# Performance work log

Hardware: AMD Instinct MI355X
Metric: run time of the kernel (lower is better)

The kernel has to match this reference:

```python
import jax, jax.numpy as jnp
import numpy as np

IN_CH = 12      # InChannels global in original code
GROWTH = 12     # growth global == growthRate
H = 34          # peptide/pseudo-sequence length (long==34 branch)
BN_EPS = 1e-5


def setup_inputs() -> dict:
    key = jax.random.key(0)
    k = jax.random.split(key, 5)
    B, C = 16384, 72  # C = IN_CH + 5*GROWTH
    x = jax.random.normal(k[0], (B, C, H, 1), dtype=jnp.float32)
    gamma = jnp.ones((C,), dtype=jnp.float32)
    beta = jnp.zeros((C,), dtype=jnp.float32)
    conv_w = jax.random.normal(k[1], (GROWTH, C, 3, 1), dtype=jnp.float32) * 0.05
    fc_w = jax.random.normal(k[2], (1, H), dtype=jnp.float32)
    fc_bias = jax.random.normal(k[3], (1,), dtype=jnp.float32)
    return {"x": x, "gamma": gamma, "beta": beta, "conv_w": conv_w,
            "fc_w": fc_w, "fc_bias": fc_bias}


def reference(x, gamma, beta, conv_w, fc_w, fc_bias):
    B, C, Hh, Ww = x.shape
    n = (C - IN_CH) // GROWTH  # number of growth groups
    sg = jax.lax.stop_gradient

    x1 = x[:, :IN_CH]                                 # [B,12,H,1]
    x2g = x[:, IN_CH:].reshape(B, n, GROWTH, Hh, 1)    # [B,n,g,H,1]

    # per-group channel means, squeezed over the width-1 axis -> [B,n,H]
    m = x2g.mean(axis=2)[..., 0]
    x11 = x1.mean(axis=1)[..., 0]                      # [B,H]

    w = fc_w[0]                                        # [H]
    lin_m = m @ w + fc_bias[0]                         # [B,n]  (bias included per F.linear call)
    lin_out = lin_m[:, -1]                             # lin(x_outt), [B]
    lin_x11 = x11 @ w + fc_bias[0]                     # [B]

    # gate for x1: sigmoid(lin(x_outt) + lin(x11)); note bias appears twice, as in torch
    g1 = jax.nn.sigmoid(lin_out + lin_x11)             # [B]
    # gates for groups 0..n-2: sigmoid(lin(group_i) + lin(x_outt))
    gates = jax.nn.sigmoid(lin_m[:, :-1] + lin_out[:, None])  # [B,n-1]

    # the expand/repeat/view dance collapses to a per-sample scalar gate broadcast
    x1g = g1[:, None, None, None] * sg(x1)             # x1 is detached in original
    # groups are appended in reversed order (i = n-2 .. 0)
    gg = gates[:, ::-1][:, :, None, None, None] * sg(x2g[:, :-1][:, ::-1])
    gg_flat = gg.reshape(B, (n - 1) * GROWTH, Hh, 1)
    x_out = x2g[:, -1]                                 # last group, appended ungated

    xxx = jnp.concatenate([x1g, gg_flat, x_out], axis=1)  # [B,C,H,1]

    # BatchNorm2d in training mode (batch statistics, biased variance)
    mu = xxx.mean(axis=(0, 2, 3), keepdims=True)
    var = xxx.var(axis=(0, 2, 3), keepdims=True)
    xn = (xxx - mu) * jax.lax.rsqrt(var + BN_EPS)
    h = jax.nn.relu(gamma[None, :, None, None] * xn + beta[None, :, None, None])

    # Conv2d(C -> GROWTH, kernel (3,1), padding (1,0), no bias)
    out = jax.lax.conv_general_dilated(
        h, conv_w, window_strides=(1, 1), padding=((1, 1), (0, 0)),
        dimension_numbers=("NCHW", "OIHW", "NCHW"))

    return jnp.concatenate([x, out], axis=1)           # [B, C+GROWTH, H, 1]
```

## Files before the change

### kernel.cpp

```cpp
#include <hip/hip_runtime.h>
#include <hip/hip_fp16.h>
#include <math.h>


#define BN_EPS 1e-5f

#define WS_S    0
#define WS_SS   72
#define WS_A    144
#define WS_B    216
#define WS_WT   288
#define WS_GATE 3744
#define K1_BLOCKS 512

typedef _Float16 f16x8 __attribute__((ext_vector_type(8)));
typedef float f32x4 __attribute__((ext_vector_type(4)));

__device__ __forceinline__ float sigmoidf_(float z) { return 1.f / (1.f + expf(-z)); }

__global__ __launch_bounds__(256) void k1_stats(const float* __restrict__ x,
                                                const float* __restrict__ fw,
                                                const float* __restrict__ fb,
                                                float* __restrict__ ws,
                                                float* __restrict__ part,
                                                int B, int nTrip)
{
    __shared__ float rs_s[3][72], rss_s[3][72], wsum_s[3][72];
    __shared__ float lm_s[3][6];
    __shared__ float sc_s[3][8];
    __shared__ float Sacc[144];

    const int tid = threadIdx.x;
    const int g = tid / 72;
    const int c = tid - g * 72;
    if (tid < 144) Sacc[tid] = 0.f;

    for (int t = blockIdx.x; t < nTrip; t += K1_BLOCKS) {
        const int b0 = t * 3;

        if (tid < 216 && b0 + g < B) {
            const float2* p = (const float2*)(x + (size_t)(b0 + g) * 2448 + c * 34);
            float rs = 0.f, rss = 0.f, wsm = 0.f;
#pragma unroll
            for (int i = 0; i < 17; ++i) {
                float2 v = p[i];
                rs += v.x + v.y;
                rss = fmaf(v.x, v.x, fmaf(v.y, v.y, rss));
                wsm = fmaf(v.x, fw[2 * i], fmaf(v.y, fw[2 * i + 1], wsm));
            }
            rs_s[g][c] = rs; rss_s[g][c] = rss; wsum_s[g][c] = wsm;
        }
        __syncthreads();

        if (tid < 18) {
            int gg = tid / 6, r = tid - gg * 6;
            float s = 0.f;
#pragma unroll
            for (int k = 0; k < 12; ++k) s += wsum_s[gg][r * 12 + k];
            lm_s[gg][r] = s * (1.f / 12.f) + fb[0];
        }
        __syncthreads();

        if (tid < 3 && b0 + tid < B) {
            float lin_out = lm_s[tid][5];
            float sc[6];
            sc[0] = sigmoidf_(lin_out + lm_s[tid][0]);
            sc[1] = sigmoidf_(lm_s[tid][4] + lin_out);
            sc[2] = sigmoidf_(lm_s[tid][3] + lin_out);
            sc[3] = sigmoidf_(lm_s[tid][2] + lin_out);
            sc[4] = sigmoidf_(lm_s[tid][1] + lin_out);
            sc[5] = 1.f;
            float* gb = ws + WS_GATE + (size_t)(b0 + tid) * 6;
#pragma unroll
            for (int r = 0; r < 6; ++r) { sc_s[tid][r] = sc[r]; gb[r] = sc[r]; }
        }
        __syncthreads();

        if (tid < 72) {
            const int r = tid / 12;
            const int dd[6] = {0, 36, 12, -12, -36, 0};
            const int src = tid + dd[r];
            float a = 0.f, q = 0.f;
#pragma unroll
            for (int gg = 0; gg < 3; ++gg) {
                if (b0 + gg < B) {
                    float s = sc_s[gg][r];
                    a = fmaf(s, rs_s[gg][src], a);
                    q = fmaf(s * s, rss_s[gg][src], q);
                }
            }
            Sacc[tid] += a; Sacc[72 + tid] += q;
        }
        __syncthreads();
    }

    if (tid < 144) part[(size_t)tid * K1_BLOCKS + blockIdx.x] = Sacc[tid];
}

__global__ __launch_bounds__(256) void k2a_reduce(float* __restrict__ ws,
                                                  const float* __restrict__ part)
{
    const int ch = blockIdx.x;
    const float* p = part + (size_t)ch * K1_BLOCKS;
    float s = 0.f;
    for (int i = threadIdx.x; i < K1_BLOCKS; i += 256) s += p[i];
#pragma unroll
    for (int off = 32; off; off >>= 1) s += __shfl_down(s, off, 64);
    __shared__ float wsum[4];
    if ((threadIdx.x & 63) == 0) wsum[threadIdx.x >> 6] = s;
    __syncthreads();
    if (threadIdx.x == 0) ws[WS_S + ch] = wsum[0] + wsum[1] + wsum[2] + wsum[3];
}

__global__ void k2b_finalize(const float* __restrict__ gamma,
                             const float* __restrict__ beta,
                             const float* __restrict__ cw,
                             float* __restrict__ ws, float invN)
{
    const int tid = threadIdx.x;
    if (tid < 72) {
        float S = ws[WS_S + tid], SS = ws[WS_SS + tid];
        float mu = S * invN;
        float var = SS * invN - mu * mu;
        float inv = rsqrtf(var + BN_EPS);
        float A = gamma[tid] * inv;
        ws[WS_A + tid] = A;
        ws[WS_B + tid] = beta[tid] - mu * A;
    }
    __half* wa = (__half*)(ws + WS_WT);
    for (int i = tid; i < 9 * 64 * 8; i += 256) {
        int j = i & 7;
        int lane = (i >> 3) & 63;
        int frag = i >> 9;
        int shift = frag / 3, ks = frag - shift * 3;
        int o = lane & 15, grp = lane >> 4;
        int ct = ks * 32 + grp * 8 + j;
        float v = (o < 12 && ct < 72) ? cw[o * 216 + ct * 3 + shift] : 0.f;
        wa[i] = __float2half(v);
    }
}

__global__ __launch_bounds__(256) void k3_out(const float* __restrict__ x,
                                              const float* __restrict__ ws,
                                              float* __restrict__ out, int B)
{
    __shared__ __align__(16) __half hs[6 * 2456];
    __shared__ float2 AB[73];
    __shared__ float gl[6][8];

    const int tid = threadIdx.x;
    const int lane = tid & 63;
    const int wid = tid >> 6;
    const int b0 = blockIdx.x * 6;
    int nb = B - b0; if (nb > 6) nb = 6;

    const __half* wa = (const __half*)(ws + WS_WT);
    f16x8 wA[9];
#pragma unroll
    for (int f = 0; f < 9; ++f)
        wA[f] = *(const f16x8*)(wa + (f * 64 + lane) * 8);

    if (tid < 73)
        AB[tid] = (tid < 72) ? make_float2(ws[WS_A + tid], ws[WS_B + tid])
                             : make_float2(0.f, 0.f);
    for (int t2 = tid; t2 < nb * 6; t2 += 256) {
        int g = t2 / 6, j = t2 - g * 6;
        gl[g][j] = ws[WS_GATE + (size_t)(b0 + g) * 6 + j];
    }
    if (tid < 24) {
        int g = tid >> 2, k = tid & 3;
        ((unsigned int*)hs)[g * 1228 + ((k < 2) ? k : (1224 + k))] = 0u;
    }
    if (nb < 6) {
        for (int i = tid; i < (6 - nb) * 1228; i += 256)
            ((unsigned int*)hs)[nb * 1228 + i] = 0u;
    }
    __syncthreads();

    for (int idx = tid; idx < nb * 612; idx += 256) {
        int g = idx / 612, v4 = idx - g * 612;
        size_t b = (size_t)(b0 + g);
        float4 q = ((const float4*)(x + b * 2448))[v4];
        ((float4*)(out + b * 2856))[v4] = q;

        const int ddc[6]  = {0, 36, 12, -12, -36, 0};
        const int sidx[6] = {0, 4, 3, 2, 1, 5};
        int rx = v4 / 102;
        int e  = v4 * 4;
        int cx0 = e / 34;
        int h0i = e - cx0 * 34;
        int dd  = ddc[rx];
        int cd0 = cx0 + dd;
        float2 ab0 = AB[cd0];
        float2 ab1 = AB[cd0 + 1];
        float s = gl[g][sidx[rx]];
        float vv[4] = {q.x, q.y, q.z, q.w};
        __half hv[4];
#pragma unroll
        for (int j = 0; j < 4; ++j) {
            float2 ab = (h0i + j >= 34) ? ab1 : ab0;
            hv[j] = __float2half(fmaxf(fmaf(ab.x * s, vv[j], ab.y), 0.f));
        }
        union { __half2 h2; unsigned int u; } pa, pb;
        pa.h2 = __halves2half2(hv[0], hv[1]);
        pb.h2 = __halves2half2(hv[2], hv[3]);
        int dst = g * 2456 + 4 + e + dd * 34;
        *reinterpret_cast<uint2*>(&hs[dst]) = make_uint2(pa.u, pb.u);
    }
    __syncthreads();

    const int sub = lane & 15, grp = lane >> 4;
    for (int t = wid; t < 13; t += 4) {
        const bool tail = (t == 12);
        int g, col;
        if (!tail) { g = t >> 1; col = (t & 1) * 16 + sub; }
        else       { g = (sub < 12) ? (sub >> 1) : 0; col = 32 + (sub & 1); }
        if (!tail && g >= nb) continue;

        const __half* hb = &hs[g * 2456 + 4];
        f32x4 acc = {0.f, 0.f, 0.f, 0.f};
        f16x8 save0, save1, save2;
        const bool needc = tail || ((t & 1) == 0);
        const int  csh   = tail ? 2 : 0;

#pragma unroll
        for (int ks = 0; ks < 3; ++ks) {
            const int cb = (ks < 2) ? (ks * 32 + grp * 8) : 64;
            const __half* hc = hb + cb * 34 + col;
#pragma unroll
            for (int sh = 0; sh < 3; ++sh) {
                f16x8 bf;
#pragma unroll
                for (int j = 0; j < 8; ++j)
                    ((unsigned short*)&bf)[j] =
                        *(const unsigned short*)(hc + j * 34 + (sh - 1));
                if (needc && sh == csh) {
                    if (ks == 0) save0 = bf;
                    else if (ks == 1) save1 = bf;
                    else save2 = bf;
                }
                acc = __builtin_amdgcn_mfma_f32_16x16x32_f16(
                          wA[sh * 3 + ks], bf, acc, 0, 0, 0);
            }
        }

        if (needc) {
            const bool m = tail ? (((sub & 1) == 1) && sub < 12) : (sub == 0);
#pragma unroll
            for (int ks = 0; ks < 3; ++ks) {
                const f16x8& sv = (ks == 0) ? save0 : (ks == 1) ? save1 : save2;
                f16x8 bt;
#pragma unroll
                for (int w = 0; w < 4; ++w)
                    ((unsigned int*)&bt)[w] =
                        m ? (((const unsigned int*)&sv)[w] ^ 0x80008000u) : 0u;
                acc = __builtin_amdgcn_mfma_f32_16x16x32_f16(
                          wA[csh * 3 + ks], bt, acc, 0, 0, 0);
            }
        }

        const bool gok = tail ? (sub < 12 && g < nb) : true;
        if (gok) {
            float* op = out + (size_t)(b0 + g) * 2856 + 2448 + col;
#pragma unroll
            for (int j = 0; j < 4; ++j) {
                int o = grp * 4 + j;
                if (o < 12) op[o * 34] = acc[j];
            }
        }
    }
}

extern "C" void kernel_launch(void* const* d_in, const int* in_sizes, int n_in,
                              void* d_out, int out_size, void* d_ws, size_t ws_size,
                              hipStream_t stream)
{
    const float* x     = (const float*)d_in[0];
    const float* gamma = (const float*)d_in[1];
    const float* beta  = (const float*)d_in[2];
    const float* cw    = (const float*)d_in[3];
    const float* fw    = (const float*)d_in[4];
    const float* fb    = (const float*)d_in[5];
    float* out = (float*)d_out;
    float* ws  = (float*)d_ws;

    const int B = in_sizes[0] / (72 * 34);
    const int nTrip = (B + 2) / 3;
    float* part = ws + WS_GATE + (size_t)B * 6;

    k1_stats<<<K1_BLOCKS, 256, 0, stream>>>(x, fw, fb, ws, part, B, nTrip);
    k2a_reduce<<<144, 256, 0, stream>>>(ws, part);
    k2b_finalize<<<1, 256, 0, stream>>>(gamma, beta, cw, ws, 1.f / ((float)B * 34.f));
    k3_out<<<(B + 5) / 6, 256, 0, stream>>>(x, ws, out, B);
}
```

Baseline: 387.3 us.

## Stage stats input via coalesced LDS loads, merge finalize kernel, enlarge grid

The stats kernel now copies each triplet of samples into shared memory with coalesced float4 loads before the per-channel reductions, replacing strided float2 global reads. The grid grows from 512 to up to 1024 blocks, capped by workspace size. The single-block finalize kernel is removed: the weight repacking moves into extra blocks of the reduce kernel, and the BN scale and shift are computed per block in the output kernel. This drops one launch and serial tail, at the cost of extra shared memory in the stats kernel and redundant per-block BN math.

```diff
diff --git a/kernel.cpp b/kernel.cpp
--- a/kernel.cpp
+++ b/kernel.cpp
@@ -7,11 +7,8 @@
 
 #define WS_S    0
 #define WS_SS   72
-#define WS_A    144
-#define WS_B    216
 #define WS_WT   288
 #define WS_GATE 3744
-#define K1_BLOCKS 512
 
 typedef _Float16 f16x8 __attribute__((ext_vector_type(8)));
 typedef float f32x4 __attribute__((ext_vector_type(4)));
@@ -25,6 +22,7 @@
                                                 float* __restrict__ part,
                                                 int B, int nTrip)
 {
+    __shared__ float xs[3 * 2448];
     __shared__ float rs_s[3][72], rss_s[3][72], wsum_s[3][72];
     __shared__ float lm_s[3][6];
     __shared__ float sc_s[3][8];
@@ -35,11 +33,20 @@
     const int c = tid - g * 72;
     if (tid < 144) Sacc[tid] = 0.f;
 
-    for (int t = blockIdx.x; t < nTrip; t += K1_BLOCKS) {
+    for (int t = blockIdx.x; t < nTrip; t += gridDim.x) {
         const int b0 = t * 3;
-
-        if (tid < 216 && b0 + g < B) {
-            const float2* p = (const float2*)(x + (size_t)(b0 + g) * 2448 + c * 34);
+        int nbt = B - b0; if (nbt > 3) nbt = 3;
+
+        {
+            const float4* xp = (const float4*)(x + (size_t)b0 * 2448);
+            const int nf4 = nbt * 612;
+            for (int i = tid; i < nf4; i += 256)
+                ((float4*)xs)[i] = xp[i];
+        }
+        __syncthreads();
+
+        if (tid < 216 && g < nbt) {
+            const float2* p = (const float2*)(xs + (g * 72 + c) * 34);
             float rs = 0.f, rss = 0.f, wsm = 0.f;
 #pragma unroll
             for (int i = 0; i < 17; ++i) {
@@ -83,7 +90,7 @@
             float a = 0.f, q = 0.f;
 #pragma unroll
             for (int gg = 0; gg < 3; ++gg) {
-                if (b0 + gg < B) {
+                if (gg < nbt) {
                     float s = sc_s[gg][r];
                     a = fmaf(s, rs_s[gg][src], a);
                     q = fmaf(s * s, rss_s[gg][src], q);
@@ -94,55 +101,77 @@
         __syncthreads();
     }
 
-    if (tid < 144) part[(size_t)tid * K1_BLOCKS + blockIdx.x] = Sacc[tid];
+    if (tid < 144) part[(size_t)tid * gridDim.x + blockIdx.x] = Sacc[tid];
 }
 
 __global__ __launch_bounds__(256) void k2a_reduce(float* __restrict__ ws,
-                                                  const float* __restrict__ part)
-{
-    const int ch = blockIdx.x;
-    const float* p = part + (size_t)ch * K1_BLOCKS;
-    float s = 0.f;
-    for (int i = threadIdx.x; i < K1_BLOCKS; i += 256) s += p[i];
-#pragma unroll
-    for (int off = 32; off; off >>= 1) s += __shfl_down(s, off, 64);
-    __shared__ float wsum[4];
-    if ((threadIdx.x & 63) == 0) wsum[threadIdx.x >> 6] = s;
-    __syncthreads();
-    if (threadIdx.x == 0) ws[WS_S + ch] = wsum[0] + wsum[1] + wsum[2] + wsum[3];
-}
-
-__global__ void k2b_finalize(const float* __restrict__ gamma,
-                             const float* __restrict__ beta,
-                             const float* __restrict__ cw,
-                             float* __restrict__ ws, float invN)
-{
-    const int tid = threadIdx.x;
-    if (tid < 72) {
-        float S = ws[WS_S + tid], SS = ws[WS_SS + tid];
-        float mu = S * invN;
-        float var = SS * invN - mu * mu;
-        float inv = rsqrtf(var + BN_EPS);
-        float A = gamma[tid] * inv;
-        ws[WS_A + tid] = A;
-        ws[WS_B + tid] = beta[tid] - mu * A;
-    }
-    __half* wa = (__half*)(ws + WS_WT);
-    for (int i = tid; i < 9 * 64 * 8; i += 256) {
-        int j = i & 7;
-        int lane = (i >> 3) & 63;
-        int frag = i >> 9;
-        int shift = frag / 3, ks = frag - shift * 3;
-        int o = lane & 15, grp = lane >> 4;
-        int ct = ks * 32 + grp * 8 + j;
-        float v = (o < 12 && ct < 72) ? cw[o * 216 + ct * 3 + shift] : 0.f;
-        wa[i] = __float2half(v);
-    }
+                                                  const float* __restrict__ part,
+                                                  const float* __restrict__ cw,
+                                                  int nblk)
+{
+    const int bid = blockIdx.x;
+    if (bid < 144) {
+        const float* p = part + (size_t)bid * nblk;
+        float s = 0.f;
+        for (int i = threadIdx.x; i < nblk; i += 256) s += p[i];
+#pragma unroll
+        for (int off = 32; off; off >>= 1) s += __shfl_down(s, off, 64);
+        __shared__ float wsum[4];
+        if ((threadIdx.x & 63) == 0) wsum[threadIdx.x >> 6] = s;
+        __syncthreads();
+        if (threadIdx.x == 0) ws[WS_S + bid] = wsum[0] + wsum[1] + wsum[2] + wsum[3];
+    } else {
+        __half* wa = (__half*)(ws + WS_WT);
+        const int base = (bid - 144) * 512;
+        for (int i = base + threadIdx.x; i < base + 512; i += 256) {
+            int j = i & 7;
+            int lane = (i >> 3) & 63;
+            int frag = i >> 9;
+            int shift = frag / 3, ks = frag - shift * 3;
+            int o = lane & 15, grp = lane >> 4;
+            int ct = ks * 32 + grp * 8 + j;
+            float v = (o < 12 && ct < 72) ? cw[o * 216 + ct * 3 + shift] : 0.f;
+            wa[i] = __float2half(v);
+        }
+    }
+}
+
+__device__ __forceinline__ void pack_h(int g, int v4, float4 q,
+                                       const float2* __restrict__ ABs,
+                                       const float* __restrict__ glf,
+                                       __half* __restrict__ hs)
+{
+    const int ddc[6]  = {0, 36, 12, -12, -36, 0};
+    const int sidx[6] = {0, 4, 3, 2, 1, 5};
+    int rx = v4 / 102;
+    int e  = v4 * 4;
+    int cx0 = e / 34;
+    int h0i = e - cx0 * 34;
+    int dd  = ddc[rx];
+    int cd0 = cx0 + dd;
+    float2 ab0 = ABs[cd0];
+    float2 ab1 = ABs[cd0 + 1];
+    float s = glf[g * 8 + sidx[rx]];
+    float vv[4] = {q.x, q.y, q.z, q.w};
+    __half hv[4];
+#pragma unroll
+    for (int j = 0; j < 4; ++j) {
+        float2 ab = (h0i + j >= 34) ? ab1 : ab0;
+        hv[j] = __float2half(fmaxf(fmaf(ab.x * s, vv[j], ab.y), 0.f));
+    }
+    union { __half2 h2; unsigned int u; } pa, pb;
+    pa.h2 = __halves2half2(hv[0], hv[1]);
+    pb.h2 = __halves2half2(hv[2], hv[3]);
+    int dst = g * 2456 + 4 + e + dd * 34;
+    *reinterpret_cast<uint2*>(&hs[dst]) = make_uint2(pa.u, pb.u);
 }
 
 __global__ __launch_bounds__(256) void k3_out(const float* __restrict__ x,
                                               const float* __restrict__ ws,
-                                              float* __restrict__ out, int B)
+                                              const float* __restrict__ gamma,
+                                              const float* __restrict__ beta,
+                                              float* __restrict__ out, int B,
+                                              float invN)
 {
     __shared__ __align__(16) __half hs[6 * 2456];
     __shared__ float2 AB[73];
@@ -160,9 +189,18 @@
     for (int f = 0; f < 9; ++f)
         wA[f] = *(const f16x8*)(wa + (f * 64 + lane) * 8);
 
-    if (tid < 73)
-        AB[tid] = (tid < 72) ? make_float2(ws[WS_A + tid], ws[WS_B + tid])
-                             : make_float2(0.f, 0.f);
+    if (tid < 73) {
+        if (tid < 72) {
+            float S = ws[WS_S + tid], SS = ws[WS_SS + tid];
+            float mu = S * invN;
+            float var = SS * invN - mu * mu;
+            float inv = rsqrtf(var + BN_EPS);
+            float A = gamma[tid] * inv;
+            AB[tid] = make_float2(A, beta[tid] - mu * A);
+        } else {
+            AB[72] = make_float2(0.f, 0.f);
+        }
+    }
     for (int t2 = tid; t2 < nb * 6; t2 += 256) {
         int g = t2 / 6, j = t2 - g * 6;
         gl[g][j] = ws[WS_GATE + (size_t)(b0 + g) * 6 + j];
@@ -177,35 +215,15 @@
     }
     __syncthreads();
 
-    for (int idx = tid; idx < nb * 612; idx += 256) {
-        int g = idx / 612, v4 = idx - g * 612;
-        size_t b = (size_t)(b0 + g);
-        float4 q = ((const float4*)(x + b * 2448))[v4];
-        ((float4*)(out + b * 2856))[v4] = q;
-
-        const int ddc[6]  = {0, 36, 12, -12, -36, 0};
-        const int sidx[6] = {0, 4, 3, 2, 1, 5};
-        int rx = v4 / 102;
-        int e  = v4 * 4;
-        int cx0 = e / 34;
-        int h0i = e - cx0 * 34;
-        int dd  = ddc[rx];
-        int cd0 = cx0 + dd;
-        float2 ab0 = AB[cd0];
-        float2 ab1 = AB[cd0 + 1];
-        float s = gl[g][sidx[rx]];
-        float vv[4] = {q.x, q.y, q.z, q.w};
-        __half hv[4];
-#pragma unroll
-        for (int j = 0; j < 4; ++j) {
-            float2 ab = (h0i + j >= 34) ? ab1 : ab0;
-            hv[j] = __float2half(fmaxf(fmaf(ab.x * s, vv[j], ab.y), 0.f));
-        }
-        union { __half2 h2; unsigned int u; } pa, pb;
-        pa.h2 = __halves2half2(hv[0], hv[1]);
-        pb.h2 = __halves2half2(hv[2], hv[3]);
-        int dst = g * 2456 + 4 + e + dd * 34;
-        *reinterpret_cast<uint2*>(&hs[dst]) = make_uint2(pa.u, pb.u);
+    {
+        const float* glf = &gl[0][0];
+        for (int idx = tid; idx < nb * 612; idx += 256) {
+            int g = idx / 612, v4 = idx - g * 612;
+            size_t b = (size_t)(b0 + g);
+            float4 q = ((const float4*)(x + b * 2448))[v4];
+            ((float4*)(out + b * 2856))[v4] = q;
+            pack_h(g, v4, q, AB, glf, hs);
+        }
     }
     __syncthreads();
 
@@ -286,10 +304,18 @@
 
     const int B = in_sizes[0] / (72 * 34);
     const int nTrip = (B + 2) / 3;
+
+    int nblk = 1024;
+    {
+        long avail = (long)(ws_size / 4) - (WS_GATE + (long)B * 6);
+        long maxblk = avail / 144;
+        if (maxblk < 1) maxblk = 1;
+        if ((long)nblk > maxblk) nblk = (int)maxblk;
+    }
     float* part = ws + WS_GATE + (size_t)B * 6;
 
-    k1_stats<<<K1_BLOCKS, 256, 0, stream>>>(x, fw, fb, ws, part, B, nTrip);
-    k2a_reduce<<<144, 256, 0, stream>>>(ws, part);
-    k2b_finalize<<<1, 256, 0, stream>>>(gamma, beta, cw, ws, 1.f / ((float)B * 34.f));
-    k3_out<<<(B + 5) / 6, 256, 0, stream>>>(x, ws, out, B);
-}
+    k1_stats<<<nblk, 256, 0, stream>>>(x, fw, fb, ws, part, B, nTrip);
+    k2a_reduce<<<153, 256, 0, stream>>>(ws, part, cw, nblk);
+    k3_out<<<(B + 5) / 6, 256, 0, stream>>>(x, ws, gamma, beta, out, B,
+                                            1.f / ((float)B * 34.f));
+}
```

Measured after the change: 385.5 us. Within noise of the previous version (-0.5%).
